# Kernel tuning notes

Hardware: AMD Instinct MI355X
Metric: run time of the kernel (lower is better)

Reference implementation:

```python
import jax, jax.numpy as jnp
import numpy as np

EPS = 1e-12


def setup_inputs() -> dict:
    key = jax.random.key(0)
    B, T, F = 16, 3000, 513
    hop, fs, t_psd = 256, 16000, 0.1
    alpha = jnp.array([1.0 - np.exp(-(hop / fs) / t_psd)], dtype=jnp.float32)
    x = jax.random.normal(key, (B, T, F), dtype=jnp.float32)
    running_mean = jnp.zeros((1, 1, F), dtype=jnp.float32)
    running_var = jnp.ones((1, 1, F), dtype=jnp.float32)
    return {"x": x, "running_mean": running_mean, "running_var": running_var, "alpha": alpha}


def reference(x, running_mean, running_var, alpha):
    # x: (B, T, F). EMA mean/var recurrence over T, then normalize.
    a = alpha.reshape(())
    B, T, F = x.shape
    m0 = jnp.broadcast_to(running_mean[:, 0, :], (B, F))
    v0 = jnp.broadcast_to(running_var[:, 0, :], (B, F))
    xt = jnp.swapaxes(x, 0, 1)  # (T, B, F)

    def step(carry, frame):
        m, v = carry
        m = (1.0 - a) * m + a * frame
        v = (1.0 - a) * v + a * (frame - m) ** 2
        return (m, v), (m, v)

    _, (means, vars_) = jax.lax.scan(step, (m0, v0), xt)
    means = jnp.swapaxes(means, 0, 1)  # (B, T, F)
    vars_ = jnp.swapaxes(vars_, 0, 1)
    return (x - means) / (vars_ * 4.0 + EPS)
```

## Files before the change

### kernel.cpp

```cpp
#include <hip/hip_runtime.h>


#define EPS 1e-12f

constexpr int B = 16;
constexpr int T = 3000;
constexpr int F = 513;
constexpr int CHUNK = 50;
constexpr int WARM = 64;
constexpr int NC = T / CHUNK;

__global__ __launch_bounds__(256)
void OnlineNorm_11982958756550_kernel(
    const float* __restrict__ x,
    const float* __restrict__ rmean,
    const float* __restrict__ rvar,
    const float* __restrict__ alpha_p,
    float* __restrict__ out)
{
    const int bf = B * F;
    const int idx = blockIdx.x * blockDim.x + threadIdx.x;
    if (idx >= bf) return;
    const int chunk = blockIdx.y;
    const int f = idx % F;
    const int b = idx / F;

    const float a = alpha_p[0];
    const float om_a = 1.0f - a;

    const int w_start = chunk * CHUNK;
    int t0 = w_start - WARM;
    float m, v;
    if (t0 <= 0) {
        t0 = 0;
        m = rmean[f];
        v = rvar[f];
    } else {
        m = 0.0f;
        v = 0.0f;
    }

    const size_t base = (size_t)b * T * F + f;
    const float* xp = x + base;
    float* op = out + base;

    #pragma unroll 8
    for (int t = t0; t < w_start; ++t) {
        const float xv = xp[(size_t)t * F];
        const float e = xv - m;
        m = fmaf(a, e, m);
        const float d = e * om_a;
        v = fmaf(a, fmaf(d, d, -v), v);
    }

    const int w_end = w_start + CHUNK;
    #pragma unroll 10
    for (int t = w_start; t < w_end; ++t) {
        const float xv = xp[(size_t)t * F];
        const float e = xv - m;
        m = fmaf(a, e, m);
        const float d = e * om_a;
        v = fmaf(a, fmaf(d, d, -v), v);
        const float denom = fmaf(v, 4.0f, EPS);
        __builtin_nontemporal_store(d * __builtin_amdgcn_rcpf(denom),
                                    &op[(size_t)t * F]);
    }
}

extern "C" void kernel_launch(void* const* d_in, const int* in_sizes, int n_in,
                              void* d_out, int out_size, void* d_ws, size_t ws_size,
                              hipStream_t stream) {
    const float* x      = (const float*)d_in[0];
    const float* rmean  = (const float*)d_in[1];
    const float* rvar   = (const float*)d_in[2];
    const float* alpha  = (const float*)d_in[3];
    float* out = (float*)d_out;

    const int bf = B * F;
    dim3 block(256);
    dim3 grid((bf + 255) / 256, NC);
    OnlineNorm_11982958756550_kernel<<<grid, block, 0, stream>>>(
        x, rmean, rvar, alpha, out);
}
```

Before: 211.6 us.

## Double-buffer row loads in the EMA scan and shrink chunk size

Result: no change. 208.4 us (-1.5%).

```diff
diff --git a/kernel.cpp b/kernel.cpp
--- a/kernel.cpp
+++ b/kernel.cpp
@@ -6,11 +6,12 @@
 constexpr int B = 16;
 constexpr int T = 3000;
 constexpr int F = 513;
-constexpr int CHUNK = 50;
+constexpr int CHUNK = 40;
 constexpr int WARM = 64;
 constexpr int NC = T / CHUNK;
+constexpr int BT = 8;
 
-__global__ __launch_bounds__(256)
+__global__ __launch_bounds__(256, 8)
 void OnlineNorm_11982958756550_kernel(
     const float* __restrict__ x,
     const float* __restrict__ rmean,
@@ -18,52 +19,70 @@
     const float* __restrict__ alpha_p,
     float* __restrict__ out)
 {
-    const int bf = B * F;
-    const int idx = blockIdx.x * blockDim.x + threadIdx.x;
-    if (idx >= bf) return;
-    const int chunk = blockIdx.y;
+    const int idx = blockIdx.x * 256 + threadIdx.x;
+    if (idx >= B * F) return;
+    const int c = blockIdx.y;
     const int f = idx % F;
     const int b = idx / F;
 
     const float a = alpha_p[0];
     const float om_a = 1.0f - a;
 
-    const int w_start = chunk * CHUNK;
+    const int w_start = c * CHUNK;
     int t0 = w_start - WARM;
     float m, v;
-    if (t0 <= 0) {
-        t0 = 0;
-        m = rmean[f];
-        v = rvar[f];
-    } else {
-        m = 0.0f;
-        v = 0.0f;
+    if (t0 <= 0) { t0 = 0; m = rmean[f]; v = rvar[f]; }
+    else         { m = 0.0f; v = 0.0f; }
+
+    const int nrows = w_start + CHUNK - t0;
+    const int nb = nrows / BT;
+    const int wb = (w_start - t0) / BT;
+
+    const size_t cs = (size_t)BT * F;
+    const float* lp = x   + (size_t)b * T * F + (size_t)t0 * F + f;
+    const float* lend = lp + (size_t)nb * cs;
+    float*       op = out + (size_t)b * T * F + (size_t)w_start * F + f;
+
+    float bufA[BT], bufB[BT];
+
+    #pragma unroll
+    for (int i = 0; i < BT; ++i) bufA[i] = lp[(size_t)i * F];
+    lp += cs;
+    if (nb > 1) {
+        #pragma unroll
+        for (int i = 0; i < BT; ++i) bufB[i] = lp[(size_t)i * F];
+        lp += cs;
     }
 
-    const size_t base = (size_t)b * T * F + f;
-    const float* xp = x + base;
-    float* op = out + base;
+    auto process = [&](float (&buf)[BT], int k) {
+        const bool is_out = (k >= wb);
+        float r[BT];
+        #pragma unroll
+        for (int i = 0; i < BT; ++i) {
+            const float e = buf[i] - m;
+            m = fmaf(a, e, m);
+            const float d = e * om_a;
+            v = fmaf(a, fmaf(d, d, -v), v);
+            if (is_out)
+                r[i] = d * __builtin_amdgcn_rcpf(fmaf(v, 4.0f, EPS));
+        }
+        if (lp < lend) {
+            #pragma unroll
+            for (int i = 0; i < BT; ++i) buf[i] = lp[(size_t)i * F];
+            lp += cs;
+        }
+        if (is_out) {
+            #pragma unroll
+            for (int i = 0; i < BT; ++i) op[(size_t)i * F] = r[i];
+            op += cs;
+        }
+    };
 
-    #pragma unroll 8
-    for (int t = t0; t < w_start; ++t) {
-        const float xv = xp[(size_t)t * F];
-        const float e = xv - m;
-        m = fmaf(a, e, m);
-        const float d = e * om_a;
-        v = fmaf(a, fmaf(d, d, -v), v);
-    }
-
-    const int w_end = w_start + CHUNK;
-    #pragma unroll 10
-    for (int t = w_start; t < w_end; ++t) {
-        const float xv = xp[(size_t)t * F];
-        const float e = xv - m;
-        m = fmaf(a, e, m);
-        const float d = e * om_a;
-        v = fmaf(a, fmaf(d, d, -v), v);
-        const float denom = fmaf(v, 4.0f, EPS);
-        __builtin_nontemporal_store(d * __builtin_amdgcn_rcpf(denom),
-                                    &op[(size_t)t * F]);
+    int k = 0;
+    while (k < nb) {
+        process(bufA, k); ++k;
+        if (k >= nb) break;
+        process(bufB, k); ++k;
     }
 }
 
```
